# Kernel optimization log

Measured on AMD Instinct MI355X. Metric: run time of the kernel, lower is better.

Reference implementation:

```python
import jax, jax.numpy as jnp
import numpy as np

INIT_SCALE = 5

def _steps(n_full):
    half = [i + 1 for i in range(0, int(n_full) + 1, 2)]
    return list(reversed(half[1:])) + half

STEP_H = np.array(_steps(192 / INIT_SCALE), dtype=np.float32)  # len 39
STEP_W = np.array(_steps(256 / INIT_SCALE), dtype=np.float32)  # len 51
MASK_H, MASK_W = len(STEP_H), len(STEP_W)


def _prelu(x, a):
    return jnp.maximum(x, 0.0) + a * jnp.minimum(x, 0.0)


def _reduce(x, w, b, a):
    # Conv2dBlock(64,4,1,1,norm='none',activation='prelu'): activation BEFORE 1x1 conv (per source)
    return jnp.einsum('nchw,oc->nohw', _prelu(x, a), w) + b[None, :, None, None]


def _crop_coords(cx, cy, H, W):
    # replicates floor(center - mask/2) / floor(center + mask/2) + border clamping
    top = cy - (MASK_H + 1) // 2
    bottom = cy + MASK_H // 2
    left = cx - (MASK_W + 1) // 2
    right = cx + MASK_W // 2
    dy1 = jnp.maximum(-top, 0)
    dy2 = jnp.maximum(bottom - H, 0)
    dx1 = jnp.maximum(-left, 0)
    dx2 = jnp.maximum(right - W, 0)
    new_top = top + dy1
    new_left = left + dx1
    new_h = jnp.maximum(bottom - dy2 - new_top, 0)
    new_w = jnp.maximum(right - dx2 - new_left, 0)
    return new_top, new_left, new_h, new_w, dy1, dx1


def _gimg(img, rows, cols):  # img (C,H,W) -> (C,len(rows),len(cols))
    return img[:, rows[:, None], cols[None, :]]


def _gmask(m, rows, cols):  # m (MASK_H,MASK_W)
    return m[rows[:, None], cols[None, :]]


def _forward(location, fea_c, fea_p, scale_param, H, W, c_landmark, p_landmark, w1, b1, a1, w2, b2, a2):
    N = fea_c.shape[0]
    ratio = H // fea_c.shape[2]
    fea_cn = _reduce(jnp.repeat(jnp.repeat(fea_c, ratio, 2), ratio, 3), w1, b1, a1)
    fea_pn = _reduce(jnp.repeat(jnp.repeat(fea_p, ratio, 2), ratio, 3), w2, b2, a2)
    C = fea_cn.shape[1]

    init_h = W / INIT_SCALE  # note: swapped vs H/W, exactly as in the original forward
    init_w = H / INIT_SCALE
    sig = jax.nn.sigmoid
    adj_cw, adj_ch = scale_param[:, :, 0, 0], scale_param[:, :, 0, 1]
    adj_pw, adj_ph = scale_param[:, :, 1, 0], scale_param[:, :, 1, 1]
    step_h = jnp.asarray(STEP_H)
    step_w = jnp.asarray(STEP_W)

    def box_mask(adj_h, adj_w):
        h = (init_h * sig(adj_h))[..., None]  # (N,32,1)
        w = (init_w * sig(adj_w))[..., None]
        return sig((h - step_h) * 2)[..., :, None] * sig((w - step_w) * 2)[..., None, :]

    src_mask = box_mask(adj_ch, adj_cw)  # (N,32,39,51)
    tar_mask = box_mask(adj_ph, adj_pw)

    r_ar = jnp.arange(MASK_H, dtype=jnp.int32)
    c_ar = jnp.arange(MASK_W, dtype=jnp.int32)
    c_cx, c_cy = c_landmark[:, :, 0], c_landmark[:, :, 1]
    p_cx, p_cy = p_landmark[:, :, 0], p_landmark[:, :, 1]
    use_lm = ~(((c_cx == 0) & (c_cy == 0)) | ((p_cx == 0) & (p_cy == 0)))  # (N,32)

    def make_patch(fea, lm_mask, cx, cy):
        top, left, nh, nw, dy1, dx1 = _crop_coords(cx, cy, H, W)
        rows = jnp.clip(top[..., None] + r_ar, 0, H - 1)        # (N,32,39)
        cols = jnp.clip(left[..., None] + c_ar, 0, W - 1)       # (N,32,51)
        mrows = jnp.clip(dy1[..., None] + r_ar, 0, MASK_H - 1)
        mcols = jnp.clip(dx1[..., None] + c_ar, 0, MASK_W - 1)
        valid = (use_lm[..., None, None]
                 & (r_ar[None, None, :, None] < nh[..., None, None])
                 & (c_ar[None, None, None, :] < nw[..., None, None]))  # (N,32,39,51)
        g = jax.vmap(lambda f, R, Cc: jax.vmap(_gimg, in_axes=(None, 0, 0))(f, R, Cc))(fea, rows, cols)  # (N,32,C,39,51)
        m = jax.vmap(jax.vmap(_gmask))(lm_mask, mrows, mcols)  # (N,32,39,51)
        patch = jnp.where(valid[:, :, None], g * m[:, :, None], 0.0)
        return patch, rows, cols, valid

    cloth, rows_c, cols_c, valid_c = make_patch(fea_cn, src_mask, c_cx, c_cy)
    person, rows_p, cols_p, valid_p = make_patch(fea_pn, tar_mask, p_cx, p_cy)

    loc5 = location.reshape(N, 32, 2, H, W)
    loc_g = jax.vmap(jax.vmap(_gimg))(loc5, rows_c, cols_c)  # (N,32,2,39,51)
    loc_patch = jnp.where(valid_c[:, :, None], loc_g, -1.0)  # -1 fill as in source

    L = MASK_H * MASK_W
    P = person.reshape(N, 32, C, L)
    K = cloth.reshape(N, 32, C, L)
    V = loc_patch.reshape(N, 32, 2, L)
    scores = jnp.einsum('nicp,nicq->nipq', P, K)  # (N,32,L,L) query=person px, key=cloth px
    corr = jax.nn.softmax(scores, axis=-1)
    flow_patch = jnp.einsum('nipq,nidq->nidp', corr, V).reshape(N, 32, 2, MASK_H, MASK_W)

    # scatter person-crop regions back into full-res outputs (invalid -> dump row/col H,W)
    rr = jnp.where(valid_p, jnp.broadcast_to(rows_p[:, :, :, None], valid_p.shape), H)
    cc = jnp.where(valid_p, jnp.broadcast_to(cols_p[:, :, None, :], valid_p.shape), W)
    bb = jnp.arange(N)[:, None, None, None]
    ii = jnp.arange(32)[None, :, None, None]
    flow_pad = jnp.full((N, 32, H + 1, W + 1, 2), -1.0, dtype=flow_patch.dtype)
    flow_pad = flow_pad.at[bb, ii, rr, cc].set(flow_patch.transpose(0, 1, 3, 4, 2))
    landmark_flow = flow_pad[:, :, :H, :W, :].transpose(0, 1, 4, 2, 3).reshape(N, 64, H, W)
    mask = jnp.zeros((N, 32, H + 1, W + 1), dtype=flow_patch.dtype).at[bb, ii, rr, cc].set(1.0)[:, :, :H, :W]
    return landmark_flow, mask


def setup_inputs() -> dict:
    key = jax.random.key(0)
    ks = jax.random.split(key, 8)
    N, H, W = 1, 192, 256
    fh, fw = H // 4, W // 4
    return {
        'location': jax.random.normal(ks[0], (N, 64, H, W), jnp.float32),
        'fea_c': jax.random.normal(ks[1], (N, 64, fh, fw), jnp.float32),
        'fea_p': jax.random.normal(ks[2], (N, 64, fh, fw), jnp.float32),
        'scale_param': jax.random.normal(ks[3], (N, 32, 2, 2), jnp.float32),
        'H': H,
        'W': W,
        'c_landmark': jax.random.randint(ks[4], (N, 32, 2), 0, 180, jnp.int32),
        'p_landmark': jax.random.randint(ks[5], (N, 32, 2), 0, 180, jnp.int32),
        'w1': jax.random.normal(ks[6], (4, 64), jnp.float32) * 0.05,
        'b1': jnp.zeros((4,), jnp.float32),
        'a1': jnp.array(0.25, jnp.float32),
        'w2': jax.random.normal(ks[7], (4, 64), jnp.float32) * 0.05,
        'b2': jnp.zeros((4,), jnp.float32),
        'a2': jnp.array(0.25, jnp.float32),
    }


def reference(location, fea_c, fea_p, scale_param, H, W, c_landmark, p_landmark, w1, b1, a1, w2, b2, a2):
    return _forward(location, fea_c, fea_p, scale_param, H, W, c_landmark, p_landmark, w1, b1, a1, w2, b2, a2)
```

## Files before the change

kernel.cpp:

```cpp
#include <hip/hip_runtime.h>

constexpr int kH = 192, kW = 256, kHW = kH * kW;
constexpr int kFH = 48, kFW = 64, kFHW = kFH * kFW;
constexpr int kMH = 39, kMW = 51;
constexpr int kL = kMH * kMW;
constexpr int kLP = 2048;
constexpr int kHeads = 32;
constexpr float kInitH = 256.0f / 5.0f;
constexpr float kInitW = 192.0f / 5.0f;
constexpr float kL2E = 1.44269504088896340736f;
constexpr float kBias = -16.0f;
constexpr float kPadCorr = 59.0f / 65536.0f;

typedef float v2f __attribute__((ext_vector_type(2)));
typedef float v8f __attribute__((ext_vector_type(8)));
#define SHPAIR(v, k) __builtin_shufflevector((v), (v), 2 * (k), 2 * (k) + 1)

__device__ __forceinline__ v2f pkfma(v2f a, v2f b, v2f c) {
  return __builtin_elementwise_fma(a, b, c);
}

__device__ __forceinline__ float fast_exp2(float x) {
#if __has_builtin(__builtin_amdgcn_exp2f)
  return __builtin_amdgcn_exp2f(x);
#else
  float r;
  asm("v_exp_f32 %0, %1\n\ts_nop 1" : "=v"(r) : "v"(x));
  return r;
#endif
}

struct HeadParams {
  int use;
  int ntop_c, nleft_c, nh_c, nw_c, dy1_c, dx1_c;
  int ntop_p, nleft_p, nh_p, nw_p, dy1_p, dx1_p;
  float h_c, w_c, h_p, w_p;
};

__device__ __forceinline__ float sigf(float x) { return 1.0f / (1.0f + __expf(-x)); }
__device__ __forceinline__ float stepH(int j) { return (float)(2 * abs(j - 19) + 1); }
__device__ __forceinline__ float stepW(int j) { return (float)(2 * abs(j - 25) + 1); }

__device__ void headParams(int i, const int* clm, const int* plm, const float* sp, HeadParams& h) {
  int ccx = clm[2 * i], ccy = clm[2 * i + 1];
  int pcx = plm[2 * i], pcy = plm[2 * i + 1];
  h.use = !(((ccx == 0) && (ccy == 0)) || ((pcx == 0) && (pcy == 0)));
  {
    int top = ccy - (kMH + 1) / 2, bottom = ccy + kMH / 2;
    int left = ccx - (kMW + 1) / 2, right = ccx + kMW / 2;
    int dy1 = max(-top, 0), dy2 = max(bottom - kH, 0);
    int dx1 = max(-left, 0), dx2 = max(right - kW, 0);
    h.ntop_c = top + dy1; h.nleft_c = left + dx1; h.dy1_c = dy1; h.dx1_c = dx1;
    h.nh_c = max(kMH - dy1 - dy2, 0); h.nw_c = max(kMW - dx1 - dx2, 0);
  }
  {
    int top = pcy - (kMH + 1) / 2, bottom = pcy + kMH / 2;
    int left = pcx - (kMW + 1) / 2, right = pcx + kMW / 2;
    int dy1 = max(-top, 0), dy2 = max(bottom - kH, 0);
    int dx1 = max(-left, 0), dx2 = max(right - kW, 0);
    h.ntop_p = top + dy1; h.nleft_p = left + dx1; h.dy1_p = dy1; h.dx1_p = dx1;
    h.nh_p = max(kMH - dy1 - dy2, 0); h.nw_p = max(kMW - dx1 - dx2, 0);
  }
  float adj_cw = sp[4 * i + 0], adj_ch = sp[4 * i + 1];
  float adj_pw = sp[4 * i + 2], adj_ph = sp[4 * i + 3];
  h.h_c = kInitH * sigf(adj_ch);
  h.w_c = kInitW * sigf(adj_cw);
  h.h_p = kInitH * sigf(adj_ph);
  h.w_p = kInitW * sigf(adj_pw);
}

__global__ void k_pre(const float* __restrict__ fc, const float* __restrict__ fp,
                      const float* __restrict__ w1, const float* __restrict__ b1, const float* __restrict__ a1,
                      const float* __restrict__ w2, const float* __restrict__ b2, const float* __restrict__ a2,
                      const float* __restrict__ sp, const int* __restrict__ clm, const int* __restrict__ plm,
                      float* __restrict__ fr, int* __restrict__ hpws) {
  int bx = blockIdx.x;
  if (bx == 24) {
    int i = threadIdx.x;
    if (i < kHeads) {
      HeadParams h; headParams(i, clm, plm, sp, h);
      int* o = hpws + i * 20;
      o[0] = h.use;
      o[1] = h.ntop_c; o[2] = h.nleft_c; o[3] = h.nh_c; o[4] = h.nw_c; o[5] = h.dy1_c; o[6] = h.dx1_c;
      o[7] = h.ntop_p; o[8] = h.nleft_p; o[9] = h.nh_p; o[10] = h.nw_p; o[11] = h.dy1_p; o[12] = h.dx1_p;
      o[13] = __float_as_int(h.h_c); o[14] = __float_as_int(h.w_c);
      o[15] = __float_as_int(h.h_p); o[16] = __float_as_int(h.w_p);
    }
    return;
  }
  int gid = bx * 256 + threadIdx.x;
  int which = gid / kFHW;
  int pix = gid - which * kFHW;
  const float* f = which ? fp : fc;
  const float* w = which ? w2 : w1;
  const float* b = which ? b2 : b1;
  float a = which ? a2[0] : a1[0];
  float acc0 = 0.f, acc1 = 0.f, acc2 = 0.f, acc3 = 0.f;
  for (int c = 0; c < 64; ++c) {
    float x = f[c * kFHW + pix];
    float pr = fmaxf(x, 0.f) + a * fminf(x, 0.f);
    acc0 = fmaf(pr, w[c], acc0);
    acc1 = fmaf(pr, w[64 + c], acc1);
    acc2 = fmaf(pr, w[128 + c], acc2);
    acc3 = fmaf(pr, w[192 + c], acc3);
  }
  float* o = fr + which * 4 * kFHW;
  o[pix]            = acc0 + b[0];
  o[kFHW + pix]     = acc1 + b[1];
  o[2 * kFHW + pix] = acc2 + b[2];
  o[3 * kFHW + pix] = acc3 + b[3];
}

__global__ void k_patch(const float* __restrict__ fr, const float* __restrict__ loc,
                        const int* __restrict__ hpws,
                        float* __restrict__ Kpl, float* __restrict__ Vpl, float4* __restrict__ Pall) {
  int i = blockIdx.y;
  int q = blockIdx.x * 256 + threadIdx.x;
  const int* hp = hpws + i * 20;
  int use = hp[0];
  int ntop_c = hp[1], nleft_c = hp[2], nh_c = hp[3], nw_c = hp[4], dy1_c = hp[5], dx1_c = hp[6];
  int ntop_p = hp[7], nleft_p = hp[8], nh_p = hp[9], nw_p = hp[10], dy1_p = hp[11], dx1_p = hp[12];
  float h_c = __int_as_float(hp[13]), w_c = __int_as_float(hp[14]);
  float h_p = __int_as_float(hp[15]), w_p = __int_as_float(hp[16]);
  int qr = q / kMW, qc = q - qr * kMW;
  constexpr int PS = kHeads * kLP;
  int o = i * kLP + q;
  {
    bool val = (q < kL) && use && (qr < nh_c) && (qc < nw_c);
    int row = min(ntop_c + qr, kH - 1);
    int col = min(nleft_c + qc, kW - 1);
    int mr = min(dy1_c + qr, kMH - 1);
    int mc = min(dx1_c + qc, kMW - 1);
    float mv = sigf((h_c - stepH(mr)) * 2.f) * sigf((w_c - stepW(mc)) * 2.f);
    int fpix = (row >> 2) * kFW + (col >> 2);
    float kx = 0.f, ky = 0.f, kz = 0.f, kw = 0.f, vx = -1.f, vy = -1.f;
    if (val) {
      kx = fr[fpix] * mv;
      ky = fr[kFHW + fpix] * mv;
      kz = fr[2 * kFHW + fpix] * mv;
      kw = fr[3 * kFHW + fpix] * mv;
      vx = loc[(2 * i) * kHW + row * kW + col];
      vy = loc[(2 * i + 1) * kHW + row * kW + col];
    }
    Kpl[o] = kx; Kpl[PS + o] = ky; Kpl[2 * PS + o] = kz; Kpl[3 * PS + o] = kw;
    Vpl[o] = vx; Vpl[PS + o] = vy;
  }
  if (q < kL) {
    bool val = use && (qr < nh_p) && (qc < nw_p);
    int row = min(ntop_p + qr, kH - 1);
    int col = min(nleft_p + qc, kW - 1);
    int mr = min(dy1_p + qr, kMH - 1);
    int mc = min(dx1_p + qc, kMW - 1);
    float mv = sigf((h_p - stepH(mr)) * 2.f) * sigf((w_p - stepW(mc)) * 2.f) * kL2E;
    int fpix = (row >> 2) * kFW + (col >> 2);
    float4 pv = make_float4(0.f, 0.f, 0.f, 0.f);
    if (val) {
      const float* frp = fr + 4 * kFHW;
      pv.x = frp[fpix] * mv;
      pv.y = frp[kFHW + fpix] * mv;
      pv.z = frp[2 * kFHW + fpix] * mv;
      pv.w = frp[3 * kFHW + fpix] * mv;
    }
    Pall[i * kL + q] = pv;
  }
}

template<int QLEN>
__global__ void __launch_bounds__(256) k_attn_t(const float* __restrict__ Kpl, const float* __restrict__ Vpl,
                                                const float4* __restrict__ Pall,
                                                float* __restrict__ pD, float* __restrict__ pX,
                                                float* __restrict__ pY) {
  constexpr int PS = kHeads * kLP;
  int i = blockIdx.z;
  int qsi = blockIdx.y;
  int p = blockIdx.x * 249 + threadIdx.x;
  int pe = min(p, kL - 1);
  const int base = i * kLP + qsi * QLEN;
  const float* kx = Kpl + base;
  const float* ky = Kpl + PS + base;
  const float* kz = Kpl + 2 * PS + base;
  const float* kw = Kpl + 3 * PS + base;
  const float* vx = Vpl + base;
  const float* vy = Vpl + PS + base;
  float4 P = Pall[i * kL + pe];
  v2f PX = {P.x, P.x}, PY = {P.y, P.y}, PZ = {P.z, P.z}, PW = {P.w, P.w};
  const v2f B = {kBias, kBias};
  v2f d0 = {0.f, 0.f}, d1 = {0.f, 0.f}, d2 = {0.f, 0.f}, d3 = {0.f, 0.f};
  v2f x0 = {0.f, 0.f}, x1 = {0.f, 0.f}, x2 = {0.f, 0.f}, x3 = {0.f, 0.f};
  v2f y0 = {0.f, 0.f}, y1 = {0.f, 0.f}, y2 = {0.f, 0.f}, y3 = {0.f, 0.f};
#pragma unroll 4
  for (int t = 0; t < QLEN; t += 8) {
    v8f Kx = *(const v8f*)(kx + t);
    v8f Ky = *(const v8f*)(ky + t);
    v8f Kz = *(const v8f*)(kz + t);
    v8f Kw = *(const v8f*)(kw + t);
    v8f Vx = *(const v8f*)(vx + t);
    v8f Vy = *(const v8f*)(vy + t);
    v2f s0 = pkfma(PW, SHPAIR(Kw, 0), B);
    v2f s1 = pkfma(PW, SHPAIR(Kw, 1), B);
    v2f s2 = pkfma(PW, SHPAIR(Kw, 2), B);
    v2f s3 = pkfma(PW, SHPAIR(Kw, 3), B);
    s0 = pkfma(PZ, SHPAIR(Kz, 0), s0);
    s1 = pkfma(PZ, SHPAIR(Kz, 1), s1);
    s2 = pkfma(PZ, SHPAIR(Kz, 2), s2);
    s3 = pkfma(PZ, SHPAIR(Kz, 3), s3);
    s0 = pkfma(PY, SHPAIR(Ky, 0), s0);
    s1 = pkfma(PY, SHPAIR(Ky, 1), s1);
    s2 = pkfma(PY, SHPAIR(Ky, 2), s2);
    s3 = pkfma(PY, SHPAIR(Ky, 3), s3);
    s0 = pkfma(PX, SHPAIR(Kx, 0), s0);
    s1 = pkfma(PX, SHPAIR(Kx, 1), s1);
    s2 = pkfma(PX, SHPAIR(Kx, 2), s2);
    s3 = pkfma(PX, SHPAIR(Kx, 3), s3);
    v2f e0 = {fast_exp2(s0.x), fast_exp2(s0.y)};
    v2f e1 = {fast_exp2(s1.x), fast_exp2(s1.y)};
    v2f e2 = {fast_exp2(s2.x), fast_exp2(s2.y)};
    v2f e3 = {fast_exp2(s3.x), fast_exp2(s3.y)};
    d0 += e0; x0 = pkfma(e0, SHPAIR(Vx, 0), x0); y0 = pkfma(e0, SHPAIR(Vy, 0), y0);
    d1 += e1; x1 = pkfma(e1, SHPAIR(Vx, 1), x1); y1 = pkfma(e1, SHPAIR(Vy, 1), y1);
    d2 += e2; x2 = pkfma(e2, SHPAIR(Vx, 2), x2); y2 = pkfma(e2, SHPAIR(Vy, 2), y2);
    d3 += e3; x3 = pkfma(e3, SHPAIR(Vx, 3), x3); y3 = pkfma(e3, SHPAIR(Vy, 3), y3);
  }
  v2f d = (d0 + d1) + (d2 + d3);
  v2f x = (x0 + x1) + (x2 + x3);
  v2f y = (y0 + y1) + (y2 + y3);
  int o = (i * gridDim.y + qsi) * kLP + pe;
  pD[o] = d.x + d.y;
  pX[o] = x.x + x.y;
  pY[o] = y.x + y.y;
}

__global__ void k_merge_full(const float* __restrict__ pD, const float* __restrict__ pX,
                             const float* __restrict__ pY, int QS,
                             const int* __restrict__ hpws, float* __restrict__ out) {
  int i = blockIdx.y;
  int pix = blockIdx.x * 256 + threadIdx.x;
  const int* hp = hpws + i * 20;
  int use = hp[0];
  int ntop_p = hp[7], nleft_p = hp[8], nh_p = hp[9], nw_p = hp[10];
  int r = pix >> 8;
  int c = pix & 255;
  int pr = r - ntop_p, pc = c - nleft_p;
  bool val = use && ((unsigned)pr < (unsigned)nh_p) && ((unsigned)pc < (unsigned)nw_p);
  float f0 = -1.f, f1 = -1.f, mk = 0.f;
  if (val) {
    int p = pr * kMW + pc;
    float den = -kPadCorr, n0 = kPadCorr, n1 = kPadCorr;
    for (int k = 0; k < QS; ++k) {
      int o = (i * QS + k) * kLP + p;
      den += pD[o]; n0 += pX[o]; n1 += pY[o];
    }
    float inv = 1.0f / den;
    f0 = n0 * inv; f1 = n1 * inv; mk = 1.0f;
  }
  out[(2 * i) * kHW + pix]      = f0;
  out[(2 * i + 1) * kHW + pix]  = f1;
  out[64 * kHW + i * kHW + pix] = mk;
}

extern "C" void kernel_launch(void* const* d_in, const int* in_sizes, int n_in,
                              void* d_out, int out_size, void* d_ws, size_t ws_size,
                              hipStream_t stream) {
  (void)in_sizes; (void)n_in; (void)out_size;
  const float* loc = (const float*)d_in[0];
  const float* fc  = (const float*)d_in[1];
  const float* fp  = (const float*)d_in[2];
  const float* sp  = (const float*)d_in[3];
  const int* clm   = (const int*)d_in[6];
  const int* plm   = (const int*)d_in[7];
  const float* w1  = (const float*)d_in[8];
  const float* b1  = (const float*)d_in[9];
  const float* a1  = (const float*)d_in[10];
  const float* w2  = (const float*)d_in[11];
  const float* b2  = (const float*)d_in[12];
  const float* a2  = (const float*)d_in[13];
  float* out = (float*)d_out;
  char* ws = (char*)d_ws;

  int*    hpws = (int*)(ws);
  float*  fr   = (float*)(ws + 4096);
  float*  Kpl  = (float*)(ws + 102400);
  float*  Vpl  = (float*)(ws + 1150976);
  float4* Pall = (float4*)(ws + 1675264);
  size_t base = 2693632;
  size_t perQS = (size_t)3 * kHeads * kLP * 4;
  int QS = 1;
  if (ws_size >= base + 16 * perQS) QS = 16;
  else if (ws_size >= base + 8 * perQS) QS = 8;
  else if (ws_size >= base + 4 * perQS) QS = 4;
  else if (ws_size >= base + 2 * perQS) QS = 2;
  float* pD = (float*)(ws + base);
  float* pX = pD + (size_t)QS * kHeads * kLP;
  float* pY = pX + (size_t)QS * kHeads * kLP;

  k_pre<<<25, 256, 0, stream>>>(fc, fp, w1, b1, a1, w2, b2, a2, sp, clm, plm, fr, hpws);
  k_patch<<<dim3(kLP / 256, kHeads), 256, 0, stream>>>(fr, loc, hpws, Kpl, Vpl, Pall);
  dim3 ag(8, QS, kHeads);
  switch (QS) {
    case 16: k_attn_t<128><<<ag, 256, 0, stream>>>(Kpl, Vpl, Pall, pD, pX, pY); break;
    case 8:  k_attn_t<256><<<ag, 256, 0, stream>>>(Kpl, Vpl, Pall, pD, pX, pY); break;
    case 4:  k_attn_t<512><<<ag, 256, 0, stream>>>(Kpl, Vpl, Pall, pD, pX, pY); break;
    case 2:  k_attn_t<1024><<<ag, 256, 0, stream>>>(Kpl, Vpl, Pall, pD, pX, pY); break;
    default: k_attn_t<2048><<<ag, 256, 0, stream>>>(Kpl, Vpl, Pall, pD, pX, pY); break;
  }
  k_merge_full<<<dim3(kHW / 256, kHeads), 256, 0, stream>>>(pD, pX, pY, QS, hpws, out);
}
```

Measured before the change: 58.12 us.

## Fuse pre-conv and head params into patch kernel; cap query splits at eight

Removes the separate k_pre launch by computing the PReLU+1x1 conv per gathered pixel inside k_patch, and computes head parameters per block into shared memory. This eliminates a kernel launch and the intermediate reduced-feature buffer, but recomputes the 64-channel conv for every patch element (many duplicates since pixels are upsampled 4x and crops overlap). It also lowers the attention loop unroll from 4 to 2 and drops the 16-way query split, using at most 8 splits.

```diff
diff --git a/kernel.cpp b/kernel.cpp
--- a/kernel.cpp
+++ b/kernel.cpp
@@ -69,62 +69,55 @@
   h.w_p = kInitW * sigf(adj_pw);
 }
 
-__global__ void k_pre(const float* __restrict__ fc, const float* __restrict__ fp,
-                      const float* __restrict__ w1, const float* __restrict__ b1, const float* __restrict__ a1,
-                      const float* __restrict__ w2, const float* __restrict__ b2, const float* __restrict__ a2,
-                      const float* __restrict__ sp, const int* __restrict__ clm, const int* __restrict__ plm,
-                      float* __restrict__ fr, int* __restrict__ hpws) {
-  int bx = blockIdx.x;
-  if (bx == 24) {
-    int i = threadIdx.x;
-    if (i < kHeads) {
-      HeadParams h; headParams(i, clm, plm, sp, h);
-      int* o = hpws + i * 20;
-      o[0] = h.use;
-      o[1] = h.ntop_c; o[2] = h.nleft_c; o[3] = h.nh_c; o[4] = h.nw_c; o[5] = h.dy1_c; o[6] = h.dx1_c;
-      o[7] = h.ntop_p; o[8] = h.nleft_p; o[9] = h.nh_p; o[10] = h.nw_p; o[11] = h.dy1_p; o[12] = h.dx1_p;
-      o[13] = __float_as_int(h.h_c); o[14] = __float_as_int(h.w_c);
-      o[15] = __float_as_int(h.h_p); o[16] = __float_as_int(h.w_p);
-    }
-    return;
-  }
-  int gid = bx * 256 + threadIdx.x;
-  int which = gid / kFHW;
-  int pix = gid - which * kFHW;
-  const float* f = which ? fp : fc;
-  const float* w = which ? w2 : w1;
-  const float* b = which ? b2 : b1;
-  float a = which ? a2[0] : a1[0];
+__device__ __forceinline__ float4 conv4(const float* __restrict__ f, const float* __restrict__ w,
+                                        const float* __restrict__ b, float a, int fpix, float s) {
   float acc0 = 0.f, acc1 = 0.f, acc2 = 0.f, acc3 = 0.f;
+#pragma unroll 8
   for (int c = 0; c < 64; ++c) {
-    float x = f[c * kFHW + pix];
+    float x = f[c * kFHW + fpix];
     float pr = fmaxf(x, 0.f) + a * fminf(x, 0.f);
     acc0 = fmaf(pr, w[c], acc0);
     acc1 = fmaf(pr, w[64 + c], acc1);
     acc2 = fmaf(pr, w[128 + c], acc2);
     acc3 = fmaf(pr, w[192 + c], acc3);
   }
-  float* o = fr + which * 4 * kFHW;
-  o[pix]            = acc0 + b[0];
-  o[kFHW + pix]     = acc1 + b[1];
-  o[2 * kFHW + pix] = acc2 + b[2];
-  o[3 * kFHW + pix] = acc3 + b[3];
-}
-
-__global__ void k_patch(const float* __restrict__ fr, const float* __restrict__ loc,
-                        const int* __restrict__ hpws,
-                        float* __restrict__ Kpl, float* __restrict__ Vpl, float4* __restrict__ Pall) {
+  return make_float4((acc0 + b[0]) * s, (acc1 + b[1]) * s, (acc2 + b[2]) * s, (acc3 + b[3]) * s);
+}
+
+__global__ void k_patch(const float* __restrict__ fc, const float* __restrict__ fp,
+                        const float* __restrict__ w1, const float* __restrict__ b1, const float* __restrict__ a1,
+                        const float* __restrict__ w2, const float* __restrict__ b2, const float* __restrict__ a2,
+                        const float* __restrict__ loc,
+                        const float* __restrict__ sp, const int* __restrict__ clm, const int* __restrict__ plm,
+                        float* __restrict__ Kpl, float* __restrict__ Vpl, float4* __restrict__ Pall,
+                        int* __restrict__ hpws) {
+  __shared__ int shp[20];
   int i = blockIdx.y;
+  if (threadIdx.x == 0) {
+    HeadParams h; headParams(i, clm, plm, sp, h);
+    shp[0] = h.use;
+    shp[1] = h.ntop_c; shp[2] = h.nleft_c; shp[3] = h.nh_c; shp[4] = h.nw_c; shp[5] = h.dy1_c; shp[6] = h.dx1_c;
+    shp[7] = h.ntop_p; shp[8] = h.nleft_p; shp[9] = h.nh_p; shp[10] = h.nw_p; shp[11] = h.dy1_p; shp[12] = h.dx1_p;
+    shp[13] = __float_as_int(h.h_c); shp[14] = __float_as_int(h.w_c);
+    shp[15] = __float_as_int(h.h_p); shp[16] = __float_as_int(h.w_p);
+    if (blockIdx.x == 0) {
+      int* o = hpws + i * 20;
+#pragma unroll
+      for (int t = 0; t < 17; ++t) o[t] = shp[t];
+    }
+  }
+  __syncthreads();
+  int use = shp[0];
+  int ntop_c = shp[1], nleft_c = shp[2], nh_c = shp[3], nw_c = shp[4], dy1_c = shp[5], dx1_c = shp[6];
+  int ntop_p = shp[7], nleft_p = shp[8], nh_p = shp[9], nw_p = shp[10], dy1_p = shp[11], dx1_p = shp[12];
+  float h_c = __int_as_float(shp[13]), w_c = __int_as_float(shp[14]);
+  float h_p = __int_as_float(shp[15]), w_p = __int_as_float(shp[16]);
+
   int q = blockIdx.x * 256 + threadIdx.x;
-  const int* hp = hpws + i * 20;
-  int use = hp[0];
-  int ntop_c = hp[1], nleft_c = hp[2], nh_c = hp[3], nw_c = hp[4], dy1_c = hp[5], dx1_c = hp[6];
-  int ntop_p = hp[7], nleft_p = hp[8], nh_p = hp[9], nw_p = hp[10], dy1_p = hp[11], dx1_p = hp[12];
-  float h_c = __int_as_float(hp[13]), w_c = __int_as_float(hp[14]);
-  float h_p = __int_as_float(hp[15]), w_p = __int_as_float(hp[16]);
   int qr = q / kMW, qc = q - qr * kMW;
   constexpr int PS = kHeads * kLP;
   int o = i * kLP + q;
+  float a1v = a1[0], a2v = a2[0];
   {
     bool val = (q < kL) && use && (qr < nh_c) && (qc < nw_c);
     int row = min(ntop_c + qr, kH - 1);
@@ -135,10 +128,8 @@
     int fpix = (row >> 2) * kFW + (col >> 2);
     float kx = 0.f, ky = 0.f, kz = 0.f, kw = 0.f, vx = -1.f, vy = -1.f;
     if (val) {
-      kx = fr[fpix] * mv;
-      ky = fr[kFHW + fpix] * mv;
-      kz = fr[2 * kFHW + fpix] * mv;
-      kw = fr[3 * kFHW + fpix] * mv;
+      float4 k = conv4(fc, w1, b1, a1v, fpix, mv);
+      kx = k.x; ky = k.y; kz = k.z; kw = k.w;
       vx = loc[(2 * i) * kHW + row * kW + col];
       vy = loc[(2 * i + 1) * kHW + row * kW + col];
     }
@@ -154,13 +145,7 @@
     float mv = sigf((h_p - stepH(mr)) * 2.f) * sigf((w_p - stepW(mc)) * 2.f) * kL2E;
     int fpix = (row >> 2) * kFW + (col >> 2);
     float4 pv = make_float4(0.f, 0.f, 0.f, 0.f);
-    if (val) {
-      const float* frp = fr + 4 * kFHW;
-      pv.x = frp[fpix] * mv;
-      pv.y = frp[kFHW + fpix] * mv;
-      pv.z = frp[2 * kFHW + fpix] * mv;
-      pv.w = frp[3 * kFHW + fpix] * mv;
-    }
+    if (val) pv = conv4(fp, w2, b2, a2v, fpix, mv);
     Pall[i * kL + q] = pv;
   }
 }
@@ -188,7 +173,7 @@
   v2f d0 = {0.f, 0.f}, d1 = {0.f, 0.f}, d2 = {0.f, 0.f}, d3 = {0.f, 0.f};
   v2f x0 = {0.f, 0.f}, x1 = {0.f, 0.f}, x2 = {0.f, 0.f}, x3 = {0.f, 0.f};
   v2f y0 = {0.f, 0.f}, y1 = {0.f, 0.f}, y2 = {0.f, 0.f}, y3 = {0.f, 0.f};
-#pragma unroll 4
+#pragma unroll 2
   for (int t = 0; t < QLEN; t += 8) {
     v8f Kx = *(const v8f*)(kx + t);
     v8f Ky = *(const v8f*)(ky + t);
@@ -278,26 +263,23 @@
   char* ws = (char*)d_ws;
 
   int*    hpws = (int*)(ws);
-  float*  fr   = (float*)(ws + 4096);
-  float*  Kpl  = (float*)(ws + 102400);
-  float*  Vpl  = (float*)(ws + 1150976);
-  float4* Pall = (float4*)(ws + 1675264);
-  size_t base = 2693632;
+  float*  Kpl  = (float*)(ws + 4096);
+  float*  Vpl  = (float*)(ws + 1052672);
+  float4* Pall = (float4*)(ws + 1576960);
+  size_t base = 2595328;
   size_t perQS = (size_t)3 * kHeads * kLP * 4;
   int QS = 1;
-  if (ws_size >= base + 16 * perQS) QS = 16;
-  else if (ws_size >= base + 8 * perQS) QS = 8;
+  if (ws_size >= base + 8 * perQS) QS = 8;
   else if (ws_size >= base + 4 * perQS) QS = 4;
   else if (ws_size >= base + 2 * perQS) QS = 2;
   float* pD = (float*)(ws + base);
   float* pX = pD + (size_t)QS * kHeads * kLP;
   float* pY = pX + (size_t)QS * kHeads * kLP;
 
-  k_pre<<<25, 256, 0, stream>>>(fc, fp, w1, b1, a1, w2, b2, a2, sp, clm, plm, fr, hpws);
-  k_patch<<<dim3(kLP / 256, kHeads), 256, 0, stream>>>(fr, loc, hpws, Kpl, Vpl, Pall);
+  k_patch<<<dim3(kLP / 256, kHeads), 256, 0, stream>>>(fc, fp, w1, b1, a1, w2, b2, a2,
+                                                       loc, sp, clm, plm, Kpl, Vpl, Pall, hpws);
   dim3 ag(8, QS, kHeads);
   switch (QS) {
-    case 16: k_attn_t<128><<<ag, 256, 0, stream>>>(Kpl, Vpl, Pall, pD, pX, pY); break;
     case 8:  k_attn_t<256><<<ag, 256, 0, stream>>>(Kpl, Vpl, Pall, pD, pX, pY); break;
     case 4:  k_attn_t<512><<<ag, 256, 0, stream>>>(Kpl, Vpl, Pall, pD, pX, pY); break;
     case 2:  k_attn_t<1024><<<ag, 256, 0, stream>>>(Kpl, Vpl, Pall, pD, pX, pY); break;
```

Result: slower. 63.05 us (+8.5%).
